# Kernel tuning notes

Measured on AMD Instinct MI355X. Metric: run time of the kernel, lower is better.

Reference implementation:

```python
import jax, jax.numpy as jnp
import numpy as np

DIM = 1024
HEADS = 16
HEAD_DIM = DIM // HEADS
SCALE = HEAD_DIM ** -0.5


def setup_inputs() -> dict:
    key = jax.random.key(0)
    k1, k2, k3 = jax.random.split(key, 3)
    x = jax.random.normal(k1, (4, 2048, DIM), dtype=jnp.float32)
    Wqkv = jax.random.normal(k2, (DIM, 3 * DIM), dtype=jnp.float32) * (DIM ** -0.5)
    Wout = jax.random.normal(k3, (DIM, DIM), dtype=jnp.float32) * (DIM ** -0.5)
    bout = jnp.zeros((DIM,), dtype=jnp.float32)
    return {"x": x, "Wqkv": Wqkv, "Wout": Wout, "bout": bout}


def reference(x, Wqkv, Wout, bout):
    b, n, _ = x.shape
    qkv = x @ Wqkv  # [b, n, 3*dim]
    q, k, v = jnp.split(qkv, 3, axis=-1)
    # [b, n, dim] -> [b, h, n, d]
    def split_heads(t):
        return t.reshape(b, n, HEADS, HEAD_DIM).transpose(0, 2, 1, 3)
    q, k, v = split_heads(q), split_heads(k), split_heads(v)
    dots = jnp.einsum('bhid,bhjd->bhij', q, k) * SCALE
    attn = jax.nn.softmax(dots, axis=-1)
    out = jnp.einsum('bhij,bhjd->bhid', attn, v)
    out = out.transpose(0, 2, 1, 3).reshape(b, n, DIM)
    return out @ Wout + bout  # dropout is identity in eval mode
```

## Files before the change

kernel.cpp:

```cpp
#include <hip/hip_runtime.h>
#include <hip/hip_bf16.h>

#define BATCH 4
#define SEQ   2048
#define DIM   1024
#define HEADS 16
#define HD    64
#define ROWS  (BATCH * SEQ)
#define QKV_N (3 * DIM)
#define ATT_C 0.18033688011f

typedef unsigned short u16;
typedef _Float16 half8 __attribute__((ext_vector_type(8)));
typedef _Float16 half4v __attribute__((ext_vector_type(4)));
typedef float f32x4 __attribute__((ext_vector_type(4)));
typedef unsigned int uint2v __attribute__((ext_vector_type(2)));

__device__ __forceinline__ void gload_lds16(const u16* g, u16* l) {
  typedef const __attribute__((address_space(1))) unsigned int* gp_t;
  typedef __attribute__((address_space(3))) unsigned int* lp_t;
  __builtin_amdgcn_global_load_lds((gp_t)(const void*)g, (lp_t)(void*)l, 16, 0, 0);
}

__global__ __launch_bounds__(256) void conv_x(const float* __restrict__ x,
                                              u16* __restrict__ xh) {
  int i = blockIdx.x * 256 + threadIdx.x;
  float4 v = ((const float4*)x)[i];
  half4v h = {(_Float16)v.x, (_Float16)v.y, (_Float16)v.z, (_Float16)v.w};
  *(half4v*)&xh[(size_t)i * 4] = h;
}

__global__ __launch_bounds__(256) void conv_w(const float* __restrict__ W,
                                              u16* __restrict__ Wt,
                                              int K, int N) {
  __shared__ float T[64][65];
  const int tid = threadIdx.x;
  const int k0 = blockIdx.y * 64, n0 = blockIdx.x * 64;
#pragma unroll
  for (int j = 0; j < 4; ++j) {
    int k = j * 16 + (tid >> 4), n4 = (tid & 15) * 4;
    float4 v = *(const float4*)(W + (size_t)(k0 + k) * N + n0 + n4);
    T[k][n4 + 0] = v.x; T[k][n4 + 1] = v.y; T[k][n4 + 2] = v.z; T[k][n4 + 3] = v.w;
  }
  __syncthreads();
#pragma unroll
  for (int j = 0; j < 4; ++j) {
    int n = j * 16 + (tid >> 4), k4 = (tid & 15) * 4;
    half4v w = {(_Float16)T[k4 + 0][n], (_Float16)T[k4 + 1][n],
                (_Float16)T[k4 + 2][n], (_Float16)T[k4 + 3][n]};
    *(half4v*)&Wt[(size_t)(n0 + n) * K + k0 + k4] = w;
  }
}

template <int MODE>
__global__ __launch_bounds__(256) void gemm_bt(
    const u16* __restrict__ A, const u16* __restrict__ Bt,
    const float* __restrict__ bias, void* __restrict__ Cv,
    u16* __restrict__ Qg, u16* __restrict__ Kg, u16* __restrict__ VtG,
    int M, int N, int K) {
  __shared__ u16 As[128 * 32];
  __shared__ u16 Bs[128 * 32];

  const int tid = threadIdx.x;
  const int wave = tid >> 6, lane = tid & 63;
  const int q4 = lane >> 4, c = lane & 15;
  const int wm = wave >> 1, wn = wave & 1;
  const int row0 = blockIdx.y * 128, col0 = blockIdx.x * 128;
  const int rr = lane >> 2, seg = lane & 3;

  f32x4 acc[4][4];
#pragma unroll
  for (int mi = 0; mi < 4; ++mi)
#pragma unroll
    for (int ni = 0; ni < 4; ++ni) acc[mi][ni] = (f32x4){0.f, 0.f, 0.f, 0.f};

  for (int k0 = 0; k0 < K; k0 += 32) {
#pragma unroll
    for (int i = 0; i < 2; ++i) {
      int chunk = wave * 2 + i;
      gload_lds16(A + (size_t)(row0 + chunk * 16 + rr) * K + k0 + seg * 8,
                  &As[chunk * 512]);
      gload_lds16(Bt + (size_t)(col0 + chunk * 16 + rr) * K + k0 + seg * 8,
                  &Bs[chunk * 512]);
    }
    __syncthreads();

    half8 af[4], bf[4];
#pragma unroll
    for (int mi = 0; mi < 4; ++mi)
      af[mi] = *(const half8*)&As[(wm * 64 + mi * 16 + c) * 32 + q4 * 8];
#pragma unroll
    for (int ni = 0; ni < 4; ++ni)
      bf[ni] = *(const half8*)&Bs[(wn * 64 + ni * 16 + c) * 32 + q4 * 8];
#pragma unroll
    for (int mi = 0; mi < 4; ++mi)
#pragma unroll
      for (int ni = 0; ni < 4; ++ni)
        acc[mi][ni] = __builtin_amdgcn_mfma_f32_16x16x32_f16(
            af[mi], bf[ni], acc[mi][ni], 0, 0, 0);
    __syncthreads();
  }

#pragma unroll
  for (int mi = 0; mi < 4; ++mi)
#pragma unroll
    for (int ni = 0; ni < 4; ++ni) {
      int colg = col0 + wn * 64 + ni * 16 + c;
      if (MODE == 0) {
        float bv = bias[colg];
#pragma unroll
        for (int r = 0; r < 4; ++r) {
          int rowg = row0 + wm * 64 + mi * 16 + q4 * 4 + r;
          ((float*)Cv)[(size_t)rowg * N + colg] = acc[mi][ni][r] + bv;
        }
      } else {
        int rowg0 = row0 + wm * 64 + mi * 16 + q4 * 4;
        int b  = rowg0 >> 11;
        int which = colg >> 10;
        int rem = colg & 1023;
        int hh = rem >> 6, d = rem & 63;
        size_t bh = (size_t)(b * HEADS + hh);
        if (which == 2) {
          int i0 = rowg0 & 2047;
          half4v pv = {(_Float16)acc[mi][ni][0], (_Float16)acc[mi][ni][1],
                       (_Float16)acc[mi][ni][2], (_Float16)acc[mi][ni][3]};
          *(half4v*)&VtG[(bh * HD + d) * SEQ + i0] = pv;
        } else {
          u16* dst = (which == 0) ? Qg : Kg;
          float sc = (which == 0) ? ATT_C : 1.0f;
#pragma unroll
          for (int r = 0; r < 4; ++r) {
            int i = (rowg0 + r) & 2047;
            ((_Float16*)dst)[(bh * SEQ + i) * HD + d] =
                (_Float16)(acc[mi][ni][r] * sc);
          }
        }
      }
    }
}

__global__ __launch_bounds__(512, 6) void attn_mfma(
    const u16* __restrict__ Qg, const u16* __restrict__ Kg,
    const u16* __restrict__ VtG, u16* __restrict__ ctx) {
  const int L  = blockIdx.x;
  const int bh = L & 63;
  const int b  = bh >> 4, h = bh & 15;
  const int qt = L >> 6;

  __shared__ u16 Ks[2][128 * 32];
  __shared__ u16 Vt[4][64 * 32];

  const int tid  = threadIdx.x;
  const int wave = tid >> 6;
  const int lane = tid & 63;
  const int q4   = lane >> 4;
  const int c    = lane & 15;
  const int rr   = lane >> 2, seg = lane & 3;
  const int sseg = seg ^ ((rr >> 1) & 3);
  const int xsw  = (q4 ^ ((c >> 1) & 3)) * 8;

  const size_t bhb = (size_t)bh;
  const int qrow0 = qt * 128 + wave * 16;

  half8 qf0 = *(const half8*)&Qg[(bhb * SEQ + qrow0 + c) * HD + q4 * 8];
  half8 qf1 = *(const half8*)&Qg[(bhb * SEQ + qrow0 + c) * HD + 32 + q4 * 8];

  f32x4 o_acc[4];
#pragma unroll
  for (int dt = 0; dt < 4; ++dt) o_acc[dt] = (f32x4){0.f, 0.f, 0.f, 0.f};
  float lp = 0.f;

  for (int j0 = 0; j0 < SEQ; j0 += 128) {
    __syncthreads();

#pragma unroll
    for (int i = 0; i < 2; ++i) {
      int chunk = wave * 2 + i;
      int kh = chunk >> 3, jr = chunk & 7;
      gload_lds16(Kg + (bhb * SEQ + j0 + jr * 16 + rr) * HD + kh * 32 + sseg * 8,
                  &Ks[kh][jr * 16 * 32]);
      int q = chunk >> 2, d16 = chunk & 3;
      gload_lds16(VtG + (bhb * HD + d16 * 16 + rr) * SEQ + j0 + q * 32 + sseg * 8,
                  &Vt[q][d16 * 16 * 32]);
    }
    __syncthreads();

#pragma unroll
    for (int kc = 0; kc < 4; ++kc) {
      const int ro0 = (kc * 32 + c) * 32 + xsw;
      const int ro1 = (kc * 32 + 16 + c) * 32 + xsw;
      half8 a00 = *(const half8*)&Ks[0][ro0];
      half8 a01 = *(const half8*)&Ks[1][ro0];
      half8 a10 = *(const half8*)&Ks[0][ro1];
      half8 a11 = *(const half8*)&Ks[1][ro1];
      f32x4 st0 = (f32x4){0.f, 0.f, 0.f, 0.f};
      f32x4 st1 = (f32x4){0.f, 0.f, 0.f, 0.f};
      st0 = __builtin_amdgcn_mfma_f32_16x16x32_f16(a00, qf0, st0, 0, 0, 0);
      st0 = __builtin_amdgcn_mfma_f32_16x16x32_f16(a01, qf1, st0, 0, 0, 0);
      st1 = __builtin_amdgcn_mfma_f32_16x16x32_f16(a10, qf0, st1, 0, 0, 0);
      st1 = __builtin_amdgcn_mfma_f32_16x16x32_f16(a11, qf1, st1, 0, 0, 0);

      float p0 = __builtin_amdgcn_exp2f(st0[0]);
      float p1 = __builtin_amdgcn_exp2f(st0[1]);
      float p2 = __builtin_amdgcn_exp2f(st0[2]);
      float p3 = __builtin_amdgcn_exp2f(st0[3]);
      float p4 = __builtin_amdgcn_exp2f(st1[0]);
      float p5 = __builtin_amdgcn_exp2f(st1[1]);
      float p6 = __builtin_amdgcn_exp2f(st1[2]);
      float p7 = __builtin_amdgcn_exp2f(st1[3]);
      lp += ((p0 + p1) + (p2 + p3)) + ((p4 + p5) + (p6 + p7));

      union { half4v h; unsigned int w[2]; } ea, eb;
      ea.h = (half4v){(_Float16)p0, (_Float16)p1, (_Float16)p2, (_Float16)p3};
      eb.h = (half4v){(_Float16)p4, (_Float16)p5, (_Float16)p6, (_Float16)p7};
      uint2v s0 = __builtin_amdgcn_permlane32_swap(ea.w[0], eb.w[0], false, false);
      uint2v s1 = __builtin_amdgcn_permlane32_swap(ea.w[1], eb.w[1], false, false);
      unsigned int A0 = s0[0], B0 = s0[1];
      unsigned int A1 = s1[0], B1 = s1[1];
      unsigned int Xs0 = __shfl_xor(A0, 16);
      unsigned int Xs1 = __shfl_xor(A1, 16);
      unsigned int Ys0 = __shfl_xor(B0, 16);
      unsigned int Ys1 = __shfl_xor(B1, 16);
      union { half8 h; unsigned int w[4]; } pb;
      const bool odd = (q4 & 1);
      pb.w[0] = odd ? Ys0 : A0;
      pb.w[1] = odd ? Ys1 : A1;
      pb.w[2] = odd ? B0  : Xs0;
      pb.w[3] = odd ? B1  : Xs1;

#pragma unroll
      for (int dt = 0; dt < 4; ++dt) {
        half8 vb = *(const half8*)&Vt[kc][(dt * 16 + c) * 32 + xsw];
        o_acc[dt] = __builtin_amdgcn_mfma_f32_16x16x32_f16(
            vb, pb.h, o_acc[dt], 0, 0, 0);
      }
    }
  }

  lp += __shfl_xor(lp, 16);
  lp += __shfl_xor(lp, 32);
  float inv = 1.0f / lp;

  size_t row = (size_t)b * SEQ + qrow0 + c;
#pragma unroll
  for (int dt = 0; dt < 4; ++dt) {
    half4v o = {(_Float16)(o_acc[dt][0] * inv), (_Float16)(o_acc[dt][1] * inv),
                (_Float16)(o_acc[dt][2] * inv), (_Float16)(o_acc[dt][3] * inv)};
    *(half4v*)&((_Float16*)ctx)[row * DIM + h * HD + dt * 16 + q4 * 4] = o;
  }
}

extern "C" void kernel_launch(void* const* d_in, const int* in_sizes, int n_in,
                              void* d_out, int out_size, void* d_ws, size_t ws_size,
                              hipStream_t stream) {
  const float* x    = (const float*)d_in[0];
  const float* Wqkv = (const float*)d_in[1];
  const float* Wout = (const float*)d_in[2];
  const float* bout = (const float*)d_in[3];
  float* out = (float*)d_out;

  u16* xh   = (u16*)d_ws;
  u16* Wqt  = xh  + (size_t)ROWS * DIM;
  u16* Wot  = Wqt + (size_t)QKV_N * DIM;
  u16* Qg   = Wot + (size_t)DIM * DIM;
  u16* Kg   = Qg  + (size_t)BATCH * HEADS * SEQ * HD;
  u16* VtG  = Kg  + (size_t)BATCH * HEADS * SEQ * HD;
  u16* ctxh = VtG + (size_t)BATCH * HEADS * HD * SEQ;

  conv_x<<<ROWS * DIM / 4 / 256, 256, 0, stream>>>(x, xh);
  conv_w<<<dim3(QKV_N / 64, DIM / 64), 256, 0, stream>>>(Wqkv, Wqt, DIM, QKV_N);
  conv_w<<<dim3(DIM / 64, DIM / 64), 256, 0, stream>>>(Wout, Wot, DIM, DIM);

  gemm_bt<1><<<dim3(QKV_N / 128, ROWS / 128), 256, 0, stream>>>(
      xh, Wqt, nullptr, nullptr, Qg, Kg, VtG, ROWS, QKV_N, DIM);

  attn_mfma<<<dim3(1024), 512, 0, stream>>>(Qg, Kg, VtG, ctxh);

  gemm_bt<0><<<dim3(DIM / 128, ROWS / 128), 256, 0, stream>>>(
      ctxh, Wot, bout, out, nullptr, nullptr, nullptr, ROWS, DIM, DIM);
}
```

Measured before the change: 303.1 us.

## Double-buffer K/V tiles in attention and compute row sums with MFMA

The attention kernel now keeps two LDS buffers for K and V^T, so the async global-to-LDS load of the next tile is issued while the current tile is computed, which halves the barriers per tile. The per-lane scalar softmax denominator and its shuffle reduction are replaced by an extra MFMA against a vector of ones, and s_setprio is raised around the MFMA groups. The launch-bounds occupancy hint is lowered. LDS per block doubles, which may cut how many blocks fit on a CU, and the row sum now accumulates fp16-rounded probabilities.

```diff
diff --git a/kernel.cpp b/kernel.cpp
--- a/kernel.cpp
+++ b/kernel.cpp
@@ -139,7 +139,7 @@
     }
 }
 
-__global__ __launch_bounds__(512, 6) void attn_mfma(
+__global__ __launch_bounds__(512, 4) void attn_mfma(
     const u16* __restrict__ Qg, const u16* __restrict__ Kg,
     const u16* __restrict__ VtG, u16* __restrict__ ctx) {
   const int L  = blockIdx.x;
@@ -147,8 +147,8 @@
   const int b  = bh >> 4, h = bh & 15;
   const int qt = L >> 6;
 
-  __shared__ u16 Ks[2][128 * 32];
-  __shared__ u16 Vt[4][64 * 32];
+  __shared__ u16 Ks[2][2][128 * 32];
+  __shared__ u16 Vt[2][4][64 * 32];
 
   const int tid  = threadIdx.x;
   const int wave = tid >> 6;
@@ -165,40 +165,47 @@
   half8 qf0 = *(const half8*)&Qg[(bhb * SEQ + qrow0 + c) * HD + q4 * 8];
   half8 qf1 = *(const half8*)&Qg[(bhb * SEQ + qrow0 + c) * HD + 32 + q4 * 8];
 
+  half8 onef;
+#pragma unroll
+  for (int i = 0; i < 8; ++i) onef[i] = (_Float16)1.0f;
+
   f32x4 o_acc[4];
 #pragma unroll
   for (int dt = 0; dt < 4; ++dt) o_acc[dt] = (f32x4){0.f, 0.f, 0.f, 0.f};
-  float lp = 0.f;
-
-  for (int j0 = 0; j0 < SEQ; j0 += 128) {
-    __syncthreads();
-
+  f32x4 l_acc = (f32x4){0.f, 0.f, 0.f, 0.f};
+
+  auto stage = [&](int jt, u16 (&KsB)[2][128 * 32], u16 (&VtB)[4][64 * 32]) {
+    const int j0 = jt * 128;
 #pragma unroll
     for (int i = 0; i < 2; ++i) {
       int chunk = wave * 2 + i;
       int kh = chunk >> 3, jr = chunk & 7;
       gload_lds16(Kg + (bhb * SEQ + j0 + jr * 16 + rr) * HD + kh * 32 + sseg * 8,
-                  &Ks[kh][jr * 16 * 32]);
+                  &KsB[kh][jr * 16 * 32]);
       int q = chunk >> 2, d16 = chunk & 3;
       gload_lds16(VtG + (bhb * HD + d16 * 16 + rr) * SEQ + j0 + q * 32 + sseg * 8,
-                  &Vt[q][d16 * 16 * 32]);
+                  &VtB[q][d16 * 16 * 32]);
     }
-    __syncthreads();
-
+  };
+
+  auto compute = [&](const u16 (&KsB)[2][128 * 32],
+                     const u16 (&VtB)[4][64 * 32]) {
 #pragma unroll
     for (int kc = 0; kc < 4; ++kc) {
       const int ro0 = (kc * 32 + c) * 32 + xsw;
       const int ro1 = (kc * 32 + 16 + c) * 32 + xsw;
-      half8 a00 = *(const half8*)&Ks[0][ro0];
-      half8 a01 = *(const half8*)&Ks[1][ro0];
-      half8 a10 = *(const half8*)&Ks[0][ro1];
-      half8 a11 = *(const half8*)&Ks[1][ro1];
+      half8 a00 = *(const half8*)&KsB[0][ro0];
+      half8 a01 = *(const half8*)&KsB[1][ro0];
+      half8 a10 = *(const half8*)&KsB[0][ro1];
+      half8 a11 = *(const half8*)&KsB[1][ro1];
       f32x4 st0 = (f32x4){0.f, 0.f, 0.f, 0.f};
       f32x4 st1 = (f32x4){0.f, 0.f, 0.f, 0.f};
+      __builtin_amdgcn_s_setprio(1);
       st0 = __builtin_amdgcn_mfma_f32_16x16x32_f16(a00, qf0, st0, 0, 0, 0);
       st0 = __builtin_amdgcn_mfma_f32_16x16x32_f16(a01, qf1, st0, 0, 0, 0);
       st1 = __builtin_amdgcn_mfma_f32_16x16x32_f16(a10, qf0, st1, 0, 0, 0);
       st1 = __builtin_amdgcn_mfma_f32_16x16x32_f16(a11, qf1, st1, 0, 0, 0);
+      __builtin_amdgcn_s_setprio(0);
 
       float p0 = __builtin_amdgcn_exp2f(st0[0]);
       float p1 = __builtin_amdgcn_exp2f(st0[1]);
@@ -208,7 +215,6 @@
       float p5 = __builtin_amdgcn_exp2f(st1[1]);
       float p6 = __builtin_amdgcn_exp2f(st1[2]);
       float p7 = __builtin_amdgcn_exp2f(st1[3]);
-      lp += ((p0 + p1) + (p2 + p3)) + ((p4 + p5) + (p6 + p7));
 
       union { half4v h; unsigned int w[2]; } ea, eb;
       ea.h = (half4v){(_Float16)p0, (_Float16)p1, (_Float16)p2, (_Float16)p3};
@@ -228,18 +234,31 @@
       pb.w[2] = odd ? B0  : Xs0;
       pb.w[3] = odd ? B1  : Xs1;
 
+      __builtin_amdgcn_s_setprio(1);
 #pragma unroll
       for (int dt = 0; dt < 4; ++dt) {
-        half8 vb = *(const half8*)&Vt[kc][(dt * 16 + c) * 32 + xsw];
+        half8 vb = *(const half8*)&VtB[kc][(dt * 16 + c) * 32 + xsw];
         o_acc[dt] = __builtin_amdgcn_mfma_f32_16x16x32_f16(
             vb, pb.h, o_acc[dt], 0, 0, 0);
       }
+      l_acc = __builtin_amdgcn_mfma_f32_16x16x32_f16(onef, pb.h, l_acc, 0, 0, 0);
+      __builtin_amdgcn_s_setprio(0);
     }
-  }
-
-  lp += __shfl_xor(lp, 16);
-  lp += __shfl_xor(lp, 32);
-  float inv = 1.0f / lp;
+  };
+
+  stage(0, Ks[0], Vt[0]);
+  __syncthreads();
+#pragma unroll 1
+  for (int t = 0; t < 16; t += 2) {
+    stage(t + 1, Ks[1], Vt[1]);
+    compute(Ks[0], Vt[0]);
+    __syncthreads();
+    if (t + 2 < 16) stage(t + 2, Ks[0], Vt[0]);
+    compute(Ks[1], Vt[1]);
+    if (t + 2 < 16) __syncthreads();
+  }
+
+  float inv = 1.0f / l_acc[0];
 
   size_t row = (size_t)b * SEQ + qrow0 + c;
 #pragma unroll
```

New measurement: 298.2 us. About the same (-1.6%).
